# Kernel optimization log

Hardware: AMD Instinct MI355X
Metric: run time of the kernel (lower is better)

The kernel has to match this reference:

```python
import jax, jax.numpy as jnp
import numpy as np

B, S, V, D, E, L = 4, 256, 50000, 300, 128, 20  # batch, seq, vocab, embed, encoder_size, labels


def _gru(x, h0, wih, whh, bih, bhh):
    """Unidirectional torch-style GRU. x: [B,S,Din], h0: [B,H]. Returns ([B,S,H], [B,H])."""
    gx = jnp.einsum('bsd,hd->bsh', x, wih) + bih  # precompute all input projections [B,S,3H]

    def step(h, gx_t):
        gh = h @ whh.T + bhh
        xr, xz, xn = jnp.split(gx_t, 3, axis=-1)
        hr, hz, hn = jnp.split(gh, 3, axis=-1)
        r = jax.nn.sigmoid(xr + hr)
        z = jax.nn.sigmoid(xz + hz)
        n = jnp.tanh(xn + r * hn)
        h2 = (1.0 - z) * n + z * h
        return h2, h2

    hT, hs = jax.lax.scan(step, h0, jnp.swapaxes(gx, 0, 1))
    return jnp.swapaxes(hs, 0, 1), hT


def _bigru(x, h0, pf, pb):
    """Bidirectional GRU. h0: [2,B,H]. Returns ([B,S,2H], [2,B,H])."""
    of, hf = _gru(x, h0[0], *pf)
    ob, hb = _gru(x[:, ::-1], h0[1], *pb)
    return jnp.concatenate([of, ob[:, ::-1]], axis=-1), jnp.stack([hf, hb])


def reference(inputs, emb,
              enc_wih_f, enc_whh_f, enc_bih_f, enc_bhh_f,
              enc_wih_b, enc_whh_b, enc_bih_b, enc_bhh_b,
              hid_wih_f, hid_whh_f, hid_bih_f, hid_bhh_f,
              hid_wih_b, hid_whh_b, hid_bih_b, hid_bhh_b,
              agg_wih_f, agg_whh_f, agg_bih_f, agg_bhh_f,
              agg_wih_b, agg_whh_b, agg_bih_b, agg_bhh_b,
              Wc1, Wc2, vc, Wb, Wd, vd, Wm, vm, Ws, vs, Wp, vp, Wpred):
    x = emb[inputs]                                # [B,S,D]
    b = x.shape[0]
    h0 = jnp.zeros((2, b, E), x.dtype)
    hp, hidden = _bigru(x, h0,
                        (enc_wih_f, enc_whh_f, enc_bih_f, enc_bhh_f),
                        (enc_wih_b, enc_whh_b, enc_bih_b, enc_bhh_b))   # [B,S,2E]
    hq, _ = _bigru(hp, hidden,
                   (hid_wih_f, hid_whh_f, hid_bih_f, hid_bhh_f),
                   (hid_wih_b, hid_whh_b, hid_bih_b, hid_bhh_b))        # [B,S,2E]

    # ptc: additive attention, score = vc . tanh(Wc1 hp_k + Wc2 hq_q)
    s1 = jnp.einsum('bkd,ed->bke', hp, Wc1)
    s2 = jnp.einsum('bqd,ed->bqe', hq, Wc2)
    sc = jnp.einsum('bqke,e->bqk', jnp.tanh(s1[:, None] + s2[:, :, None]), vc)
    ptc = jnp.einsum('bqk,bkd->bqd', jax.nn.softmax(sc, -1), hp)

    # ptb: bilinear attention, score = hq_q . (Wb hp_k)
    sc = jnp.einsum('bqd,bkd->bqk', hq, jnp.einsum('bkd,ed->bke', hp, Wb))
    ptb = jnp.einsum('bqk,bkd->bqd', jax.nn.softmax(sc, -1), hp)

    # ptd: score = vd . tanh(Wd (hp_k * hq_q))
    sc = jnp.einsum('bqke,e->bqk', jnp.tanh(jnp.einsum('bqkd,ed->bqke', hp[:, None] * hq[:, :, None], Wd)), vd)
    ptd = jnp.einsum('bqk,bkd->bqd', jax.nn.softmax(sc, -1), hp)

    # ptm: score = vm . tanh(Wm (hp_k - hq_q))
    sc = jnp.einsum('bqke,e->bqk', jnp.tanh(jnp.einsum('bqkd,ed->bqke', hp[:, None] - hq[:, :, None], Wm)), vm)
    ptm = jnp.einsum('bqk,bkd->bqd', jax.nn.softmax(sc, -1), hp)

    # pts: self, score = vs . tanh(Ws (hq_k * hq_q))
    sc = jnp.einsum('bqke,e->bqk', jnp.tanh(jnp.einsum('bqkd,ed->bqke', hq[:, None] * hq[:, :, None], Ws)), vs)
    pts = jnp.einsum('bqk,bkd->bqd', jax.nn.softmax(sc, -1), hq)

    agg = jnp.concatenate([hq, pts, ptc, ptd, ptb, ptm], axis=-1)  # [B,S,12E]
    agg_rep, _ = _bigru(agg, jnp.zeros((2, b, E), x.dtype),
                        (agg_wih_f, agg_whh_f, agg_bih_f, agg_bhh_f),
                        (agg_wih_b, agg_whh_b, agg_bih_b, agg_bhh_b))  # [B,S,2E]

    # pooled query rl over hq
    sj = jnp.einsum('bse,e->bs', jnp.tanh(jnp.einsum('bsd,ed->bse', hq, Wp)), vp)
    rl = jnp.einsum('bs,bsd->bd', jax.nn.softmax(sj, -1), hq)       # [B,2E]

    # final pooling over agg_rep (note: no tanh here, matching source)
    sc = jnp.einsum('bse,e->bs',
                    jnp.einsum('bsd,ed->bse', agg_rep, Wc1) + jnp.einsum('bd,ed->be', rl, Wc2)[:, None],
                    vc)
    rr = jnp.einsum('bs,bsd->bd', jax.nn.softmax(sc, -1), agg_rep)  # [B,2E]
    return jax.nn.sigmoid(rr @ Wpred.T)                              # [B,labels]


def setup_inputs() -> dict:
    key = jax.random.key(0)
    ks = iter(jax.random.split(key, 64))
    f = lambda *s: jax.random.normal(next(ks), s, jnp.float32) * 0.05
    H3 = 3 * E
    return dict(
        inputs=jax.random.randint(next(ks), (B, S), 0, V),
        emb=f(V, D),
        enc_wih_f=f(H3, D), enc_whh_f=f(H3, E), enc_bih_f=f(H3), enc_bhh_f=f(H3),
        enc_wih_b=f(H3, D), enc_whh_b=f(H3, E), enc_bih_b=f(H3), enc_bhh_b=f(H3),
        hid_wih_f=f(H3, 2 * E), hid_whh_f=f(H3, E), hid_bih_f=f(H3), hid_bhh_f=f(H3),
        hid_wih_b=f(H3, 2 * E), hid_whh_b=f(H3, E), hid_bih_b=f(H3), hid_bhh_b=f(H3),
        agg_wih_f=f(H3, 12 * E), agg_whh_f=f(H3, E), agg_bih_f=f(H3), agg_bhh_f=f(H3),
        agg_wih_b=f(H3, 12 * E), agg_whh_b=f(H3, E), agg_bih_b=f(H3), agg_bhh_b=f(H3),
        Wc1=f(E, 2 * E), Wc2=f(E, 2 * E), vc=f(E),
        Wb=f(2 * E, 2 * E),
        Wd=f(E, 2 * E), vd=f(E),
        Wm=f(E, 2 * E), vm=f(E),
        Ws=f(E, 2 * E), vs=f(E),
        Wp=f(E, 2 * E), vp=f(E),
        Wpred=f(L, 2 * E),
    )
```

## Files before the change

### kernel.cpp

```cpp
#include <hip/hip_runtime.h>
#include <math.h>

#define BB 4
#define SS 256
#define DD 300
#define DP 304
#define EE 128
#define LL 20
#define H3 384
#define D2 256
#define D12 1536

typedef __attribute__((ext_vector_type(8)))  short short8;
typedef __attribute__((ext_vector_type(16))) float f32x16;

__device__ __forceinline__ float tanh_fast(float x){
  float e = __expf(2.f*x);
  return 1.f - 2.f/(e+1.f);
}
__device__ __forceinline__ float sigmoidf_(float x){ return 1.f/(1.f+__expf(-x)); }
__device__ __forceinline__ float bf16_to_f(unsigned u){ return __builtin_bit_cast(float, u<<16); }
__device__ __forceinline__ float bf16hi_to_f(unsigned u){ return __builtin_bit_cast(float, u & 0xFFFF0000u); }
__device__ __forceinline__ unsigned bf16_rne(float f){
  unsigned u = __builtin_bit_cast(unsigned, f);
  return (u + 0x7FFFu + ((u>>16)&1u)) >> 16;
}
__device__ __forceinline__ unsigned pack_bf16x2(float lo, float hi){
  return bf16_rne(lo) | (bf16_rne(hi)<<16);
}

__global__ void k_cvt_bf16(const float* __restrict__ src, unsigned short* __restrict__ dst, int n2){
  int i = blockIdx.x*blockDim.x + threadIdx.x;
  if (i < n2){
    float2 f = *(const float2*)(src + 2*i);
    *(unsigned*)(dst + 2*i) = pack_bf16x2(f.x, f.y);
  }
}

struct CvtSeg { const float* src; unsigned short* dst; int rows, Ks, Kd; };
struct CvtArgs { CvtSeg s[13]; };
__global__ void k_cvt_weights(CvtArgs a){
  CvtSeg sg = a.s[blockIdx.y];
  int p = blockIdx.x*256 + threadIdx.x;
  int Kd2 = sg.Kd>>1;
  int npairs = sg.rows*Kd2;
  if (p >= npairs) return;
  int row = p/Kd2, kk = (p - row*Kd2)*2;
  float f0 = (kk   < sg.Ks)? sg.src[(size_t)row*sg.Ks+kk  ] : 0.f;
  float f1 = (kk+1 < sg.Ks)? sg.src[(size_t)row*sg.Ks+kk+1] : 0.f;
  *(unsigned*)(sg.dst + (size_t)row*sg.Kd + kk) = pack_bf16x2(f0,f1);
}

__global__ void k_embed(const int* __restrict__ inp, const float* __restrict__ emb,
                        unsigned short* __restrict__ xb){
  int row = blockIdx.x;
  int idx = inp[row];
  const float* src = emb + (size_t)idx*DD;
  unsigned short* dst = xb + (size_t)row*DP;
  int p = threadIdx.x;
  if (p < DP/2){
    float f0 = (2*p   < DD)? src[2*p  ] : 0.f;
    float f1 = (2*p+1 < DD)? src[2*p+1] : 0.f;
    *(unsigned*)(dst + 2*p) = pack_bf16x2(f0,f1);
  }
}

__global__ void k_init2(float* __restrict__ gf, const float* __restrict__ bf,
                        float* __restrict__ gb, const float* __restrict__ bb){
  int row = blockIdx.x, n = threadIdx.x;
  gf[(size_t)row*H3+n] = bf[n];
  gb[(size_t)row*H3+n] = bb[n];
}

__global__ __launch_bounds__(64) void k_mmbf(
    const unsigned short* __restrict__ X, const unsigned short* __restrict__ W,
    const float* __restrict__ bias, float* __restrict__ out,
    int N, int K, int kspan){
  int lane=threadIdx.x, col=lane&31, half=lane>>5;
  int n0=blockIdx.x*32, m0=blockIdx.y*64;
  int ks=blockIdx.z*kspan, ke=ks+kspan; if (ke>K) ke=K;
  const unsigned short* pa0 = X + (size_t)(m0+col)*K + half*8;
  const unsigned short* pa1 = pa0 + (size_t)32*K;
  const unsigned short* pb  = W + (size_t)(n0+col)*K + half*8;
  f32x16 acc0={}, acc1={};
  #pragma unroll 2
  for (int k=ks;k<ke;k+=16){
    short8 a0=__builtin_bit_cast(short8, *(const uint4*)(pa0+k));
    short8 a1=__builtin_bit_cast(short8, *(const uint4*)(pa1+k));
    short8 bv=__builtin_bit_cast(short8, *(const uint4*)(pb +k));
    acc0=__builtin_amdgcn_mfma_f32_32x32x16_bf16(a0,bv,acc0,0,0,0);
    acc1=__builtin_amdgcn_mfma_f32_32x32x16_bf16(a1,bv,acc1,0,0,0);
  }
  int cn = n0+col;
  if (gridDim.z==1){
    float bn = bias? bias[cn] : 0.f;
    #pragma unroll
    for (int r=0;r<16;r++){
      int row=(r&3)+8*(r>>2)+4*half;
      out[(size_t)(m0+row)*N+cn]    = acc0[r]+bn;
      out[(size_t)(m0+32+row)*N+cn] = acc1[r]+bn;
    }
  } else {
    #pragma unroll
    for (int r=0;r<16;r++){
      int row=(r&3)+8*(r>>2)+4*half;
      atomicAdd(&out[(size_t)(m0+row)*N+cn],    acc0[r]);
      atomicAdd(&out[(size_t)(m0+32+row)*N+cn], acc1[r]);
    }
  }
}

__global__ __launch_bounds__(512, 2) void k_gru_scan(const float* __restrict__ gxf, const float* __restrict__ gxb,
                          const float* __restrict__ whhf, const float* __restrict__ whhb,
                          const float* __restrict__ bhhf, const float* __restrict__ bhhb,
                          const float* __restrict__ h0,
                          float* __restrict__ out,
                          float* __restrict__ hT){
  int b=blockIdx.x, dir=blockIdx.y, tid=threadIdx.x;
  const float* gx  = dir? gxb : gxf;
  const float* whh = dir? whhb : whhf;
  const float* bhh = dir? bhhb : bhhf;
  int r = tid>>2, part = tid&3, phase = r&7;
  float4 w_r[8], w_z[8], w_n[8];
  #pragma unroll
  for (int j=0;j<8;j++){
    int jj=(j+phase)&7;
    int off = part*32 + jj*4;
    w_r[j] = *(const float4*)&whh[(size_t)r*EE        + off];
    w_z[j] = *(const float4*)&whh[(size_t)(r+128)*EE  + off];
    w_n[j] = *(const float4*)&whh[(size_t)(r+256)*EE  + off];
  }
  float b_r=bhh[r], b_z=bhh[r+128], b_n=bhh[r+256];
  __shared__ __align__(16) float h[2][EE];
  float hprev = h0? h0[((size_t)dir*BB+b)*EE + r] : 0.f;
  if (part==0) h[0][r] = hprev;
  float xr=0.f,xz=0.f,xn=0.f;
  {
    int s0 = dir? (SS-1) : 0;
    const float* g0 = gx + ((size_t)b*SS+s0)*H3;
    if (part==0){ xr=g0[r]; xz=g0[EE+r]; xn=g0[2*EE+r]; }
  }
  __syncthreads();
  int cur=0;
  for (int t=0;t<SS;t++){
    int s = dir? (SS-1-t) : t;
    float ar=0.f, az=0.f, an=0.f;
    #pragma unroll
    for (int j=0;j<8;j++){
      int jj=(j+phase)&7;
      float4 hv = *(const float4*)&h[cur][part*32 + jj*4];
      ar += w_r[j].x*hv.x + w_r[j].y*hv.y + w_r[j].z*hv.z + w_r[j].w*hv.w;
      az += w_z[j].x*hv.x + w_z[j].y*hv.y + w_z[j].z*hv.z + w_z[j].w*hv.w;
      an += w_n[j].x*hv.x + w_n[j].y*hv.y + w_n[j].z*hv.z + w_n[j].w*hv.w;
    }
    ar += __shfl_xor(ar,1); ar += __shfl_xor(ar,2);
    az += __shfl_xor(az,1); az += __shfl_xor(az,2);
    an += __shfl_xor(an,1); an += __shfl_xor(an,2);
    if (part==0){
      float rg = sigmoidf_(xr + ar + b_r);
      float zg = sigmoidf_(xz + az + b_z);
      float ng = tanh_fast(xn + rg*(an + b_n));
      float h2 = (1.f-zg)*ng + zg*hprev;
      hprev = h2;
      h[cur^1][r] = h2;
      out[((size_t)b*SS+s)*D2 + dir*EE + r] = h2;
      if (t+1<SS){
        int sn = dir? (SS-2-t) : (t+1);
        const float* gn = gx + ((size_t)b*SS+sn)*H3;
        xr=gn[r]; xz=gn[EE+r]; xn=gn[2*EE+r];
      }
    }
    cur^=1;
    __syncthreads();
  }
  if (hT && part==0) hT[((size_t)dir*BB+b)*EE+r]=hprev;
}

__global__ void k_copy_hq(const unsigned short* __restrict__ hqb, unsigned short* __restrict__ aggb){
  int row=blockIdx.x;
  aggb[(size_t)row*D12 + threadIdx.x] = hqb[(size_t)row*D2 + threadIdx.x];
}

__device__ __forceinline__ void softmax256(float val, float* red, float* p){
  int tid=threadIdx.x;
  red[tid]=val; __syncthreads();
  for (int st=128; st>0; st>>=1){ if (tid<st) red[tid]=fmaxf(red[tid],red[tid+st]); __syncthreads(); }
  float mx=red[0]; __syncthreads();
  float ex=__expf(val-mx); red[tid]=ex; __syncthreads();
  for (int st=128; st>0; st>>=1){ if (tid<st) red[tid]+=red[tid+st]; __syncthreads(); }
  float inv=1.f/red[0];
  p[tid]=ex*inv; __syncthreads();
}

__global__ __launch_bounds__(256) void k_attn_add(const float* __restrict__ A, const float* __restrict__ Bq,
                          const float* __restrict__ v, float sign,
                          const float* __restrict__ V, unsigned short* __restrict__ aggout, int off){
  __shared__ __align__(16) float bq[EE];
  __shared__ __align__(16) float vv[EE];
  __shared__ float p[SS]; __shared__ float red[SS];
  int q=blockIdx.x, b=blockIdx.y, tid=threadIdx.x;
  if (tid<EE){ bq[tid]=sign*Bq[((size_t)b*SS+q)*EE+tid]; vv[tid]=v[tid]; }
  __syncthreads();
  const float* Ar = A + ((size_t)b*SS+tid)*EE;
  float s=0.f;
  #pragma unroll
  for (int e=0;e<EE;e+=4){
    float4 a=*(const float4*)(Ar+e);
    float4 bb=*(const float4*)(bq+e);
    float4 vw=*(const float4*)(vv+e);
    s += vw.x*tanh_fast(a.x+bb.x)+vw.y*tanh_fast(a.y+bb.y)+vw.z*tanh_fast(a.z+bb.z)+vw.w*tanh_fast(a.w+bb.w);
  }
  softmax256(s, red, p);
  const float* V0 = V + (size_t)b*SS*D2;
  float o=0.f;
  for (int k=0;k<SS;k++) o += p[k]*V0[(size_t)k*D2+tid];
  aggout[((size_t)b*SS+q)*D12 + off + tid] = (unsigned short)bf16_rne(o);
}

__global__ __launch_bounds__(256) void k_attn_bil(const float* __restrict__ Pb, const float* __restrict__ hq,
                          const float* __restrict__ V, unsigned short* __restrict__ aggout, int off){
  __shared__ __align__(16) float hqq[D2];
  __shared__ float p[SS]; __shared__ float red[SS];
  int q=blockIdx.x, b=blockIdx.y, tid=threadIdx.x;
  hqq[tid]=hq[((size_t)b*SS+q)*D2+tid];
  __syncthreads();
  const float* Pr = Pb + ((size_t)b*SS+tid)*D2;
  float s=0.f;
  #pragma unroll
  for (int d=0;d<D2;d+=4){
    float4 a=*(const float4*)(Pr+d);
    float4 hh=*(const float4*)(hqq+d);
    s += a.x*hh.x+a.y*hh.y+a.z*hh.z+a.w*hh.w;
  }
  softmax256(s, red, p);
  const float* V0 = V + (size_t)b*SS*D2;
  float o=0.f;
  for (int k=0;k<SS;k++) o += p[k]*V0[(size_t)k*D2+tid];
  aggout[((size_t)b*SS+q)*D12 + off + tid] = (unsigned short)bf16_rne(o);
}

__global__ __launch_bounds__(256, 2) void k_mulattn_fused(
    const unsigned short* __restrict__ keysb,
    const float* __restrict__ qm,
    const unsigned short* __restrict__ Wb,
    const float* __restrict__ v,
    const float* __restrict__ V,
    unsigned short* __restrict__ aggout, int off){
  __shared__ __align__(16) float qrow[D2];
  __shared__ __align__(16) float vrow[EE];
  __shared__ float scq[SS];
  __shared__ float red[SS];
  __shared__ float p[SS];
  int q=blockIdx.x, b=blockIdx.y, tid=threadIdx.x;
  int wave=tid>>6, lane=tid&63;
  size_t bS = (size_t)b*SS;
  qrow[tid]=qm[(bS+q)*D2+tid];
  if (tid<EE) vrow[tid]=v[tid];
  __syncthreads();

  f32x16 acc[2][4]={};
  int m0 = wave*64;
  int col = lane&31, half = lane>>5;
  const unsigned short* krow0 = keysb + (bS + m0 + col)*D2 + half*8;
  const unsigned short* krow1 = krow0 + 32*D2;
  const unsigned short* wrow[4];
  #pragma unroll
  for (int n=0;n<4;n++) wrow[n] = Wb + (size_t)(n*32+col)*D2 + half*8;

  for (int d0=0; d0<D2; d0+=16){
    float4 qsA = *(const float4*)&qrow[d0 + half*8];
    float4 qsB = *(const float4*)&qrow[d0 + half*8 + 4];
    short8 bfrag[4];
    #pragma unroll
    for (int n=0;n<4;n++) bfrag[n] = __builtin_bit_cast(short8, *(const uint4*)(wrow[n]+d0));
    #pragma unroll
    for (int i=0;i<2;i++){
      uint4 raw = *(const uint4*)((i? krow1:krow0) + d0);
      float f0=bf16_to_f(raw.x)*qsA.x, f1=bf16hi_to_f(raw.x)*qsA.y;
      float f2=bf16_to_f(raw.y)*qsA.z, f3=bf16hi_to_f(raw.y)*qsA.w;
      float f4=bf16_to_f(raw.z)*qsB.x, f5=bf16hi_to_f(raw.z)*qsB.y;
      float f6=bf16_to_f(raw.w)*qsB.z, f7=bf16hi_to_f(raw.w)*qsB.w;
      uint4 pk;
      pk.x=pack_bf16x2(f0,f1);
      pk.y=pack_bf16x2(f2,f3);
      pk.z=pack_bf16x2(f4,f5);
      pk.w=pack_bf16x2(f6,f7);
      short8 afrag = __builtin_bit_cast(short8, pk);
      #pragma unroll
      for (int n=0;n<4;n++)
        acc[i][n] = __builtin_amdgcn_mfma_f32_32x32x16_bf16(afrag, bfrag[n], acc[i][n], 0,0,0);
    }
  }
  float vn[4];
  #pragma unroll
  for (int n=0;n<4;n++) vn[n]=vrow[n*32+col];
  #pragma unroll
  for (int i=0;i<2;i++){
    #pragma unroll
    for (int r=0;r<16;r++){
      float s = vn[0]*tanh_fast(acc[i][0][r]) + vn[1]*tanh_fast(acc[i][1][r])
              + vn[2]*tanh_fast(acc[i][2][r]) + vn[3]*tanh_fast(acc[i][3][r]);
      s += __shfl_xor(s,1,32); s += __shfl_xor(s,2,32); s += __shfl_xor(s,4,32);
      s += __shfl_xor(s,8,32); s += __shfl_xor(s,16,32);
      int k = m0 + i*32 + (r&3) + 8*(r>>2) + 4*half;
      scq[k] = s;
    }
  }
  __syncthreads();
  float val = scq[tid];
  softmax256(val, red, p);
  const float* V0 = V + bS*D2;
  float o=0.f;
  for (int k=0;k<SS;k++) o += p[k]*V0[(size_t)k*D2+tid];
  aggout[(bS+q)*D12 + off + tid] = (unsigned short)bf16_rne(o);
}

__global__ __launch_bounds__(256) void k_rl(const float* __restrict__ spj, const float* __restrict__ hq,
                    const float* __restrict__ vp, const float* __restrict__ Wc2,
                    float* __restrict__ sB){
  __shared__ __align__(16) float vpl[EE];
  __shared__ float p[SS]; __shared__ float red[SS];
  __shared__ __align__(16) float rr[D2];
  int b=blockIdx.x, tid=threadIdx.x;
  if (tid<EE) vpl[tid]=vp[tid];
  __syncthreads();
  const float* row = spj + ((size_t)b*SS+tid)*EE;
  float sj=0.f;
  #pragma unroll
  for (int e=0;e<EE;e+=4){
    float4 a=*(const float4*)(row+e);
    float4 vw=*(const float4*)(vpl+e);
    sj += vw.x*tanh_fast(a.x)+vw.y*tanh_fast(a.y)+vw.z*tanh_fast(a.z)+vw.w*tanh_fast(a.w);
  }
  softmax256(sj, red, p);
  float o=0.f;
  for (int s=0;s<SS;s++) o += p[s]*hq[((size_t)b*SS+s)*D2+tid];
  rr[tid]=o; __syncthreads();
  if (tid<EE){
    const float* wr = Wc2 + (size_t)tid*D2;
    float a=0.f;
    #pragma unroll
    for (int d=0;d<D2;d+=4){
      float4 w4=*(const float4*)(wr+d);
      float4 r4=*(const float4*)(rr+d);
      a += w4.x*r4.x+w4.y*r4.y+w4.z*r4.z+w4.w*r4.w;
    }
    sB[(size_t)b*EE+tid]=a;
  }
}

__global__ __launch_bounds__(256) void k_final(const float* __restrict__ sA, const float* __restrict__ sB,
                       const float* __restrict__ vc, const float* __restrict__ agg_rep,
                       const float* __restrict__ Wpred, float* __restrict__ out){
  __shared__ __align__(16) float sBl[EE];
  __shared__ __align__(16) float vcl[EE];
  __shared__ float p[SS]; __shared__ float red[SS]; __shared__ float rr[D2];
  int b=blockIdx.x, tid=threadIdx.x;
  if (tid<EE){ sBl[tid]=sB[(size_t)b*EE+tid]; vcl[tid]=vc[tid]; }
  __syncthreads();
  const float* rowA = sA + ((size_t)b*SS+tid)*EE;
  float sc=0.f;
  #pragma unroll
  for (int e=0;e<EE;e+=4){
    float4 a=*(const float4*)(rowA+e);
    float4 bb=*(const float4*)(sBl+e);
    float4 vw=*(const float4*)(vcl+e);
    sc += vw.x*(a.x+bb.x)+vw.y*(a.y+bb.y)+vw.z*(a.z+bb.z)+vw.w*(a.w+bb.w);
  }
  softmax256(sc, red, p);
  float o=0.f;
  for (int s=0;s<SS;s++) o += p[s]*agg_rep[((size_t)b*SS+s)*D2+tid];
  rr[tid]=o; __syncthreads();
  if (tid<LL){
    float a=0.f;
    const float* wr = Wpred + (size_t)tid*D2;
    for (int d=0;d<D2;d++) a += wr[d]*rr[d];
    out[(size_t)b*LL+tid]=sigmoidf_(a);
  }
}

extern "C" void kernel_launch(void* const* d_in, const int* in_sizes, int n_in,
                              void* d_out, int out_size, void* d_ws, size_t ws_size,
                              hipStream_t stream){
  (void)in_sizes; (void)n_in; (void)out_size; (void)ws_size;
  const int*   inp = (const int*)d_in[0];
  const float* emb = (const float*)d_in[1];
  const float* enc_wih_f=(const float*)d_in[2],  *enc_whh_f=(const float*)d_in[3],
             *enc_bih_f=(const float*)d_in[4],  *enc_bhh_f=(const float*)d_in[5];
  const float* enc_wih_b=(const float*)d_in[6],  *enc_whh_b=(const float*)d_in[7],
             *enc_bih_b=(const float*)d_in[8],  *enc_bhh_b=(const float*)d_in[9];
  const float* hid_wih_f=(const float*)d_in[10], *hid_whh_f=(const float*)d_in[11],
             *hid_bih_f=(const float*)d_in[12], *hid_bhh_f=(const float*)d_in[13];
  const float* hid_wih_b=(const float*)d_in[14], *hid_whh_b=(const float*)d_in[15],
             *hid_bih_b=(const float*)d_in[16], *hid_bhh_b=(const float*)d_in[17];
  const float* agg_wih_f=(const float*)d_in[18], *agg_whh_f=(const float*)d_in[19],
             *agg_bih_f=(const float*)d_in[20], *agg_bhh_f=(const float*)d_in[21];
  const float* agg_wih_b=(const float*)d_in[22], *agg_whh_b=(const float*)d_in[23],
             *agg_bih_b=(const float*)d_in[24], *agg_bhh_b=(const float*)d_in[25];
  const float* Wc1=(const float*)d_in[26], *Wc2=(const float*)d_in[27], *vc=(const float*)d_in[28];
  const float* Wb =(const float*)d_in[29];
  const float* Wd =(const float*)d_in[30], *vd=(const float*)d_in[31];
  const float* Wm =(const float*)d_in[32], *vm=(const float*)d_in[33];
  const float* Ws =(const float*)d_in[34], *vs=(const float*)d_in[35];
  const float* Wp =(const float*)d_in[36], *vp=(const float*)d_in[37];
  const float* Wpred=(const float*)d_in[38];

  float* ws = (float*)d_ws;
  size_t o = 0;
  float* gxf     = ws + o; o += (size_t)BB*SS*H3;
  float* gxb     = ws + o; o += (size_t)BB*SS*H3;
  float* hp      = ws + o; o += (size_t)BB*SS*D2;
  float* hq      = ws + o; o += (size_t)BB*SS*D2;
  float* hidden  = ws + o; o += (size_t)2*BB*EE;
  float* s1      = ws + o; o += (size_t)BB*SS*EE;
  float* s2      = ws + o; o += (size_t)BB*SS*EE;
  float* Am      = ws + o; o += (size_t)BB*SS*EE;
  float* Bm      = ws + o; o += (size_t)BB*SS*EE;
  float* Pb      = ws + o; o += (size_t)BB*SS*D2;
  float* spj     = ws + o; o += (size_t)BB*SS*EE;
  float* agg_rep = ws + o; o += (size_t)BB*SS*D2;
  float* sA      = ws + o; o += (size_t)BB*SS*EE;
  float* sB      = ws + o; o += (size_t)BB*EE;
  unsigned short* x_bf      = (unsigned short*)(ws+o); o += (size_t)BB*SS*DP/2;
  unsigned short* hp_bf     = (unsigned short*)(ws+o); o += (size_t)BB*SS*D2/2;
  unsigned short* hq_bf     = (unsigned short*)(ws+o); o += (size_t)BB*SS*D2/2;
  unsigned short* agg_bf    = (unsigned short*)(ws+o); o += (size_t)BB*SS*D12/2;
  unsigned short* aggrep_bf = (unsigned short*)(ws+o); o += (size_t)BB*SS*D2/2;
  unsigned short* encf_bf   = (unsigned short*)(ws+o); o += (size_t)H3*DP/2;
  unsigned short* encb_bf   = (unsigned short*)(ws+o); o += (size_t)H3*DP/2;
  unsigned short* hidf_bf   = (unsigned short*)(ws+o); o += (size_t)H3*D2/2;
  unsigned short* hidb_bf   = (unsigned short*)(ws+o); o += (size_t)H3*D2/2;
  unsigned short* aggf_bf   = (unsigned short*)(ws+o); o += (size_t)H3*D12/2;
  unsigned short* aggb_bf   = (unsigned short*)(ws+o); o += (size_t)H3*D12/2;
  unsigned short* Wc1_bf    = (unsigned short*)(ws+o); o += (size_t)EE*D2/2;
  unsigned short* Wc2_bf    = (unsigned short*)(ws+o); o += (size_t)EE*D2/2;
  unsigned short* Wm_bf     = (unsigned short*)(ws+o); o += (size_t)EE*D2/2;
  unsigned short* Wb_bf     = (unsigned short*)(ws+o); o += (size_t)D2*D2/2;
  unsigned short* Wp_bf     = (unsigned short*)(ws+o); o += (size_t)EE*D2/2;
  unsigned short* Wd_bf     = (unsigned short*)(ws+o); o += (size_t)EE*D2/2;
  unsigned short* Ws_bf     = (unsigned short*)(ws+o); o += (size_t)EE*D2/2;

  const int M = BB*SS;
  auto mmbf=[&](const unsigned short* X,const unsigned short* W,const float* bias,
                float* outp,int N,int K,int z,int kspan){
    dim3 g(N/32, M/64, z);
    k_mmbf<<<g,64,0,stream>>>(X,W,bias,outp,N,K,kspan);
  };

  k_embed<<<M,256,0,stream>>>(inp, emb, x_bf);
  CvtArgs ca;
  ca.s[0]  = {enc_wih_f, encf_bf, H3, DD, DP};
  ca.s[1]  = {enc_wih_b, encb_bf, H3, DD, DP};
  ca.s[2]  = {hid_wih_f, hidf_bf, H3, D2, D2};
  ca.s[3]  = {hid_wih_b, hidb_bf, H3, D2, D2};
  ca.s[4]  = {agg_wih_f, aggf_bf, H3, D12, D12};
  ca.s[5]  = {agg_wih_b, aggb_bf, H3, D12, D12};
  ca.s[6]  = {Wc1, Wc1_bf, EE, D2, D2};
  ca.s[7]  = {Wc2, Wc2_bf, EE, D2, D2};
  ca.s[8]  = {Wm,  Wm_bf,  EE, D2, D2};
  ca.s[9]  = {Wb,  Wb_bf,  D2, D2, D2};
  ca.s[10] = {Wp,  Wp_bf,  EE, D2, D2};
  ca.s[11] = {Wd,  Wd_bf,  EE, D2, D2};
  ca.s[12] = {Ws,  Ws_bf,  EE, D2, D2};
  {
    int maxpairs = H3*D12/2;
    dim3 g((maxpairs+255)/256, 13);
    k_cvt_weights<<<g,256,0,stream>>>(ca);
  }

  k_init2<<<M,H3,0,stream>>>(gxf, enc_bih_f, gxb, enc_bih_b);
  mmbf(x_bf, encf_bf, nullptr, gxf, H3, DP, 4, 80);
  mmbf(x_bf, encb_bf, nullptr, gxb, H3, DP, 4, 80);
  k_gru_scan<<<dim3(BB,2),512,0,stream>>>(gxf,gxb,enc_whh_f,enc_whh_b,enc_bhh_f,enc_bhh_b,
                                          nullptr,hp,hidden);
  k_cvt_bf16<<<(M*D2/2+255)/256,256,0,stream>>>(hp, hp_bf, M*D2/2);

  k_init2<<<M,H3,0,stream>>>(gxf, hid_bih_f, gxb, hid_bih_b);
  mmbf(hp_bf, hidf_bf, nullptr, gxf, H3, D2, 4, 64);
  mmbf(hp_bf, hidb_bf, nullptr, gxb, H3, D2, 4, 64);
  k_gru_scan<<<dim3(BB,2),512,0,stream>>>(gxf,gxb,hid_whh_f,hid_whh_b,hid_bhh_f,hid_bhh_b,
                                          hidden,hq,nullptr);
  k_cvt_bf16<<<(M*D2/2+255)/256,256,0,stream>>>(hq, hq_bf, M*D2/2);

  mmbf(hp_bf, Wc1_bf, nullptr, s1,  EE, D2, 1, D2);
  mmbf(hq_bf, Wc2_bf, nullptr, s2,  EE, D2, 1, D2);
  mmbf(hp_bf, Wm_bf,  nullptr, Am,  EE, D2, 1, D2);
  mmbf(hq_bf, Wm_bf,  nullptr, Bm,  EE, D2, 1, D2);
  mmbf(hp_bf, Wb_bf,  nullptr, Pb,  D2, D2, 1, D2);
  mmbf(hq_bf, Wp_bf,  nullptr, spj, EE, D2, 1, D2);

  k_copy_hq<<<M,256,0,stream>>>(hq_bf, agg_bf);
  dim3 gq(SS,BB);
  k_attn_add<<<gq,256,0,stream>>>(s1,s2,vc, 1.f, hp, agg_bf, 512);
  k_attn_add<<<gq,256,0,stream>>>(Am,Bm,vm,-1.f, hp, agg_bf, 1280);
  k_attn_bil<<<gq,256,0,stream>>>(Pb,hq,hp,agg_bf,1024);
  k_mulattn_fused<<<gq,256,0,stream>>>(hp_bf,hq,Wd_bf,vd,hp,agg_bf,768);
  k_mulattn_fused<<<gq,256,0,stream>>>(hq_bf,hq,Ws_bf,vs,hq,agg_bf,256);

  k_init2<<<M,H3,0,stream>>>(gxf, agg_bih_f, gxb, agg_bih_b);
  mmbf(agg_bf, aggf_bf, nullptr, gxf, H3, D12, 8, 192);
  mmbf(agg_bf, aggb_bf, nullptr, gxb, H3, D12, 8, 192);
  k_gru_scan<<<dim3(BB,2),512,0,stream>>>(gxf,gxb,agg_whh_f,agg_whh_b,agg_bhh_f,agg_bhh_b,
                                          nullptr,agg_rep,nullptr);
  k_cvt_bf16<<<(M*D2/2+255)/256,256,0,stream>>>(agg_rep, aggrep_bf, M*D2/2);

  k_rl<<<BB,256,0,stream>>>(spj,hq,vp,Wc2,sB);
  mmbf(aggrep_bf, Wc1_bf, nullptr, sA, EE, D2, 1, D2);
  k_final<<<BB,256,0,stream>>>(sA,sB,vc,agg_rep,Wpred,(float*)d_out);
}
```

Measured before the change: 1.180 ms.

## Restructure GRU scan to two threads per gate row with shared dot buffer

The recurrent GRU scan changes from 512 threads (4 lanes per hidden unit, each computing all three gates) to 768 threads, where each pair of threads computes one of the 384 gate-row dot products over half of h. The dots go to shared memory, and 128 threads then combine the gates. This cuts the per-thread serial FMA chain and the shuffle reductions, but adds a second __syncthreads per timestep and a shared-memory round trip. The single h buffer is now safe because the extra barrier separates reads from writes.

```diff
diff --git a/kernel.cpp b/kernel.cpp
--- a/kernel.cpp
+++ b/kernel.cpp
@@ -110,7 +110,8 @@
   }
 }
 
-__global__ __launch_bounds__(512, 2) void k_gru_scan(const float* __restrict__ gxf, const float* __restrict__ gxb,
+__global__ __launch_bounds__(768, 3) void k_gru_scan(
+                          const float* __restrict__ gxf, const float* __restrict__ gxb,
                           const float* __restrict__ whhf, const float* __restrict__ whhb,
                           const float* __restrict__ bhhf, const float* __restrict__ bhhb,
                           const float* __restrict__ h0,
@@ -120,60 +121,65 @@
   const float* gx  = dir? gxb : gxf;
   const float* whh = dir? whhb : whhf;
   const float* bhh = dir? bhhb : bhhf;
-  int r = tid>>2, part = tid&3, phase = r&7;
-  float4 w_r[8], w_z[8], w_n[8];
-  #pragma unroll
-  for (int j=0;j<8;j++){
-    int jj=(j+phase)&7;
-    int off = part*32 + jj*4;
-    w_r[j] = *(const float4*)&whh[(size_t)r*EE        + off];
-    w_z[j] = *(const float4*)&whh[(size_t)(r+128)*EE  + off];
-    w_n[j] = *(const float4*)&whh[(size_t)(r+256)*EE  + off];
-  }
-  float b_r=bhh[r], b_z=bhh[r+128], b_n=bhh[r+256];
-  __shared__ __align__(16) float h[2][EE];
-  float hprev = h0? h0[((size_t)dir*BB+b)*EE + r] : 0.f;
-  if (part==0) h[0][r] = hprev;
-  float xr=0.f,xz=0.f,xn=0.f;
+  int g = tid>>1, half = tid&1;
+
+  float4 w[16];
   {
+    const float* wr = whh + (size_t)g*EE + half*64;
+    #pragma unroll
+    for (int j=0;j<16;j++) w[j] = *(const float4*)(wr + j*4);
+  }
+
+  __shared__ __align__(16) float hsh[EE];
+  __shared__ float dots[H3];
+
+  bool comb = (tid < EE);
+  float hprev=0.f, b_r=0.f, b_z=0.f, b_n=0.f, xr=0.f, xz=0.f, xn=0.f;
+  if (comb){
+    int r = tid;
+    b_r = bhh[r]; b_z = bhh[r+EE]; b_n = bhh[r+2*EE];
+    hprev = h0? h0[((size_t)dir*BB+b)*EE + r] : 0.f;
+    hsh[r] = hprev;
     int s0 = dir? (SS-1) : 0;
     const float* g0 = gx + ((size_t)b*SS+s0)*H3;
-    if (part==0){ xr=g0[r]; xz=g0[EE+r]; xn=g0[2*EE+r]; }
-  }
-  __syncthreads();
-  int cur=0;
+    xr=g0[r]; xz=g0[r+EE]; xn=g0[r+2*EE];
+  }
+  __syncthreads();
+
+  const float* hb = hsh + half*64;
   for (int t=0;t<SS;t++){
-    int s = dir? (SS-1-t) : t;
-    float ar=0.f, az=0.f, an=0.f;
-    #pragma unroll
-    for (int j=0;j<8;j++){
-      int jj=(j+phase)&7;
-      float4 hv = *(const float4*)&h[cur][part*32 + jj*4];
-      ar += w_r[j].x*hv.x + w_r[j].y*hv.y + w_r[j].z*hv.z + w_r[j].w*hv.w;
-      az += w_z[j].x*hv.x + w_z[j].y*hv.y + w_z[j].z*hv.z + w_z[j].w*hv.w;
-      an += w_n[j].x*hv.x + w_n[j].y*hv.y + w_n[j].z*hv.z + w_n[j].w*hv.w;
-    }
-    ar += __shfl_xor(ar,1); ar += __shfl_xor(ar,2);
-    az += __shfl_xor(az,1); az += __shfl_xor(az,2);
-    an += __shfl_xor(an,1); an += __shfl_xor(an,2);
-    if (part==0){
+    float a0=0.f,a1=0.f,a2=0.f,a3=0.f;
+    #pragma unroll
+    for (int j=0;j<16;j++){
+      float4 hv = *(const float4*)(hb + j*4);
+      a0 += w[j].x*hv.x; a1 += w[j].y*hv.y;
+      a2 += w[j].z*hv.z; a3 += w[j].w*hv.w;
+    }
+    float a = (a0+a1)+(a2+a3);
+    a += __shfl_xor(a, 1);
+    if (!half) dots[g] = a;
+    __syncthreads();
+
+    if (comb){
+      int r = tid;
+      int s = dir? (SS-1-t) : t;
+      float ar=dots[r], az=dots[r+EE], an=dots[r+2*EE];
       float rg = sigmoidf_(xr + ar + b_r);
       float zg = sigmoidf_(xz + az + b_z);
       float ng = tanh_fast(xn + rg*(an + b_n));
       float h2 = (1.f-zg)*ng + zg*hprev;
       hprev = h2;
-      h[cur^1][r] = h2;
+      hsh[r] = h2;
       out[((size_t)b*SS+s)*D2 + dir*EE + r] = h2;
       if (t+1<SS){
         int sn = dir? (SS-2-t) : (t+1);
         const float* gn = gx + ((size_t)b*SS+sn)*H3;
-        xr=gn[r]; xz=gn[EE+r]; xn=gn[2*EE+r];
+        xr=gn[r]; xz=gn[r+EE]; xn=gn[r+2*EE];
       }
     }
-    cur^=1;
     __syncthreads();
   }
-  if (hT && part==0) hT[((size_t)dir*BB+b)*EE+r]=hprev;
+  if (hT && comb) hT[((size_t)dir*BB+b)*EE+tid]=hprev;
 }
 
 __global__ void k_copy_hq(const unsigned short* __restrict__ hqb, unsigned short* __restrict__ aggb){
@@ -471,14 +477,14 @@
   k_init2<<<M,H3,0,stream>>>(gxf, enc_bih_f, gxb, enc_bih_b);
   mmbf(x_bf, encf_bf, nullptr, gxf, H3, DP, 4, 80);
   mmbf(x_bf, encb_bf, nullptr, gxb, H3, DP, 4, 80);
-  k_gru_scan<<<dim3(BB,2),512,0,stream>>>(gxf,gxb,enc_whh_f,enc_whh_b,enc_bhh_f,enc_bhh_b,
+  k_gru_scan<<<dim3(BB,2),768,0,stream>>>(gxf,gxb,enc_whh_f,enc_whh_b,enc_bhh_f,enc_bhh_b,
                                           nullptr,hp,hidden);
   k_cvt_bf16<<<(M*D2/2+255)/256,256,0,stream>>>(hp, hp_bf, M*D2/2);
 
   k_init2<<<M,H3,0,stream>>>(gxf, hid_bih_f, gxb, hid_bih_b);
   mmbf(hp_bf, hidf_bf, nullptr, gxf, H3, D2, 4, 64);
   mmbf(hp_bf, hidb_bf, nullptr, gxb, H3, D2, 4, 64);
-  k_gru_scan<<<dim3(BB,2),512,0,stream>>>(gxf,gxb,hid_whh_f,hid_whh_b,hid_bhh_f,hid_bhh_b,
+  k_gru_scan<<<dim3(BB,2),768,0,stream>>>(gxf,gxb,hid_whh_f,hid_whh_b,hid_bhh_f,hid_bhh_b,
                                           hidden,hq,nullptr);
   k_cvt_bf16<<<(M*D2/2+255)/256,256,0,stream>>>(hq, hq_bf, M*D2/2);
 
@@ -500,7 +506,7 @@
   k_init2<<<M,H3,0,stream>>>(gxf, agg_bih_f, gxb, agg_bih_b);
   mmbf(agg_bf, aggf_bf, nullptr, gxf, H3, D12, 8, 192);
   mmbf(agg_bf, aggb_bf, nullptr, gxb, H3, D12, 8, 192);
-  k_gru_scan<<<dim3(BB,2),512,0,stream>>>(gxf,gxb,agg_whh_f,agg_whh_b,agg_bhh_f,agg_bhh_b,
+  k_gru_scan<<<dim3(BB,2),768,0,stream>>>(gxf,gxb,agg_whh_f,agg_whh_b,agg_bhh_f,agg_bhh_b,
                                           nullptr,agg_rep,nullptr);
   k_cvt_bf16<<<(M*D2/2+255)/256,256,0,stream>>>(agg_rep, aggrep_bf, M*D2/2);
 
```

Measured after the change: 1.393 ms. 1.18x slower.
